# Optimization experiments

Measured on AMD Instinct MI355X. Metric: run time of the kernel, lower is better.

Reference implementation:

```python
import jax, jax.numpy as jnp
import numpy as np

N_USER = 27094
M_SPOT = 42852
N_EDGE = 2_000_000
D_FEAT = 128


def setup_inputs() -> dict:
    key = jax.random.key(0)
    k1, k2, k3, k4 = jax.random.split(key, 4)
    spot_x = jax.random.normal(k1, (M_SPOT, D_FEAT), dtype=jnp.float32)
    user_x = jax.random.normal(k2, (N_USER, D_FEAT), dtype=jnp.float32)
    u_idx = jax.random.randint(k3, (N_EDGE,), 0, N_USER, dtype=jnp.int32)
    s_idx = jax.random.randint(k4, (N_EDGE,), 0, M_SPOT, dtype=jnp.int32)
    user_spot = jnp.stack([u_idx, s_idx], axis=0)  # [2, E]
    return {"spot_x": spot_x, "user_x": user_x, "user_spot": user_spot}


def reference(spot_x, user_x, user_spot):
    u = user_spot[0]  # [E] user index per edge
    s = user_spot[1]  # [E] spot index per edge
    # symmetric GCN normalization: 1/sqrt(deg_u * deg_s) per edge
    user_deg = jnp.bincount(u, length=N_USER)
    spot_deg = jnp.bincount(s, length=M_SPOT)
    div = jnp.sqrt((user_deg[u] * spot_deg[s]).astype(spot_x.dtype))[:, None]  # [E,1]
    # spot -> user aggregation
    source_spot = spot_x[s] / div                                   # [E, D]
    user_out = jax.ops.segment_sum(source_spot, u, num_segments=N_USER)
    # user -> spot aggregation
    source_user = user_x[u] / div                                   # [E, D]
    spot_out = jax.ops.segment_sum(source_user, s, num_segments=M_SPOT)
    return (spot_out, user_out)
```

## Files before the change

kernel.cpp:

```cpp
#include <hip/hip_runtime.h>
#include <stdint.h>


#define NPB_LOG2 6
#define NPB 64
#define MAXB 768
#define PART_CHUNK 2048
#define BH_CHUNK 16384
#define SORT_CAP 8192
#define CSCAN_CH 256

__device__ __forceinline__ ushort f2bf(float f) {
    uint32_t u = __float_as_uint(f);
    return (ushort)((u + 0x7fffu + ((u >> 16) & 1u)) >> 16);
}

__global__ __launch_bounds__(256) void bhist_kernel(
        const int* __restrict__ u, const int* __restrict__ s, int E,
        int nbu, int nbs, int* __restrict__ bd) {
    __shared__ int hist[2 * MAXB];
    const int tid = threadIdx.x;
    const int nb = nbu + nbs;
    const int beg = blockIdx.x * BH_CHUNK;
    const int end = min(beg + BH_CHUNK, E);
    for (int b = tid; b < nb; b += 256) hist[b] = 0;
    __syncthreads();
    for (int i = beg + tid; i < end; i += 256) {
        atomicAdd(&hist[u[i] >> NPB_LOG2], 1);
        atomicAdd(&hist[nbu + (s[i] >> NPB_LOG2)], 1);
    }
    __syncthreads();
    for (int b = tid; b < nb; b += 256) {
        int h = hist[b];
        if (h) atomicAdd(&bd[b], h);
    }
}

__global__ __launch_bounds__(1024) void scan2_kernel(
        const int* __restrict__ bd, int nbu, int nbs,
        int* __restrict__ buoff, int* __restrict__ bsoff,
        int* __restrict__ gcu, int* __restrict__ gcs) {
    __shared__ int wsums[16];
    __shared__ int total;
    const int tid = threadIdx.x, lane = tid & 63, wid = tid >> 6;
    const int n   = blockIdx.x ? nbs : nbu;
    const int* in = blockIdx.x ? (bd + nbu) : bd;
    int* out = blockIdx.x ? bsoff : buoff;
    int* gc  = blockIdx.x ? gcs   : gcu;
    int v = (tid < n) ? in[tid] : 0;
    int x = v;
#pragma unroll
    for (int d = 1; d < 64; d <<= 1) {
        int t = __shfl_up(x, d);
        if (lane >= d) x += t;
    }
    if (lane == 63) wsums[wid] = x;
    __syncthreads();
    if (tid == 0) {
        int run = 0;
#pragma unroll
        for (int w = 0; w < 16; ++w) { int t = wsums[w]; wsums[w] = run; run += t; }
        total = run;
    }
    __syncthreads();
    int excl = wsums[wid] + (x - v);
    if (tid < n) { out[tid] = excl; gc[tid] = excl; }
    if (tid == 0) out[n] = total;
}

__global__ void convert_kernel(const float* __restrict__ x, const float* __restrict__ isd,
                               ushort* __restrict__ xb, int n_rows) {
    int idx = blockIdx.x * blockDim.x + threadIdx.x;
    if (idx >= (n_rows << 6)) return;
    int row = idx >> 6, c = idx & 63;
    float w = isd[row];
    const float* xr = x + ((size_t)row << 7);
    ushort2 o;
    o.x = f2bf(xr[c] * w);
    o.y = f2bf(xr[c + 64] * w);
    *reinterpret_cast<ushort2*>(xb + ((size_t)row << 7) + 2 * c) = o;
}

__global__ __launch_bounds__(256) void part_kernel(
        const int* __restrict__ prim, const int* __restrict__ sec, int E,
        int nb, int* __restrict__ gcur, uint32_t* __restrict__ out) {
    __shared__ int hist[MAXB];
    __shared__ int loff[MAXB];
    __shared__ int gbase[MAXB];
    __shared__ int cur[MAXB];
    __shared__ int wsum[4];
    __shared__ uint32_t sbuf[PART_CHUNK];
    const int tid = threadIdx.x;
    const int lane = tid & 63;
    const int wid = tid >> 6;
    const int beg = blockIdx.x * PART_CHUNK;
    const int end = min(beg + PART_CHUNK, E);
    const int cnt_total = end - beg;
    for (int b = tid; b < nb; b += 256) hist[b] = 0;
    __syncthreads();
    for (int i = beg + tid; i < end; i += 256)
        atomicAdd(&hist[prim[i] >> NPB_LOG2], 1);
    __syncthreads();
    {
        int b0 = tid * 3;
        int h0 = (b0 + 0 < nb) ? hist[b0 + 0] : 0;
        int h1 = (b0 + 1 < nb) ? hist[b0 + 1] : 0;
        int h2 = (b0 + 2 < nb) ? hist[b0 + 2] : 0;
        int tsum = h0 + h1 + h2;
        int x = tsum;
#pragma unroll
        for (int d = 1; d < 64; d <<= 1) {
            int t = __shfl_up(x, d);
            if (lane >= d) x += t;
        }
        if (lane == 63) wsum[wid] = x;
        __syncthreads();
        if (tid == 0) {
            int run = 0;
#pragma unroll
            for (int w = 0; w < 4; ++w) { int t = wsum[w]; wsum[w] = run; run += t; }
        }
        __syncthreads();
        int base = wsum[wid] + (x - tsum);
        if (b0 + 0 < nb) loff[b0 + 0] = base;
        if (b0 + 1 < nb) loff[b0 + 1] = base + h0;
        if (b0 + 2 < nb) loff[b0 + 2] = base + h0 + h1;
    }
    __syncthreads();
    for (int b = tid; b < nb; b += 256) {
        cur[b] = loff[b];
        int c = hist[b];
        gbase[b] = c > 0 ? atomicAdd(&gcur[b], c) : 0;
    }
    __syncthreads();
    for (int i = beg + tid; i < end; i += 256) {
        int p = prim[i], s = sec[i];
        int b = p >> NPB_LOG2;
        int l = atomicAdd(&cur[b], 1);
        sbuf[l] = ((uint32_t)p << 16) | (uint32_t)s;
    }
    __syncthreads();
    for (int k = tid; k < cnt_total; k += 256) {
        uint32_t p = sbuf[k];
        int b = (int)(p >> (16 + NPB_LOG2));
        out[gbase[b] + (k - loff[b])] = p;
    }
}

__global__ __launch_bounds__(256) void bdeg_kernel(
        const uint32_t* __restrict__ buf, const int* __restrict__ boff,
        float* __restrict__ isd, int n_rows) {
    __shared__ int hist[NPB];
    const int tid = threadIdx.x;
    const int jbeg = boff[blockIdx.x];
    const int cnt = boff[blockIdx.x + 1] - jbeg;
    if (tid < NPB) hist[tid] = 0;
    __syncthreads();
    for (int k = tid; k < cnt; k += 256)
        atomicAdd(&hist[(buf[jbeg + k] >> 16) & (NPB - 1)], 1);
    __syncthreads();
    if (tid < NPB) {
        int node = (blockIdx.x << NPB_LOG2) + tid;
        if (node < n_rows) {
            int h = hist[tid];
            isd[node] = h > 0 ? rsqrtf((float)h) : 0.f;
        }
    }
}

__global__ __launch_bounds__(512) void fscan_kernel(
        const ushort* __restrict__ xb, const uint32_t* __restrict__ buf,
        const int* __restrict__ boff, float* __restrict__ isd_out,
        float* __restrict__ out, int n_rows) {
    __shared__ uint32_t sorted[SORT_CAP];
    __shared__ int hist[NPB];
    __shared__ int scur[NPB];
    __shared__ float isdl[NPB];
    const int tid = threadIdx.x;
    const int jbeg = boff[blockIdx.x];
    const int cnt = boff[blockIdx.x + 1] - jbeg;
    if (cnt <= 0) {
        if (tid < NPB) {
            int node = (blockIdx.x << NPB_LOG2) + tid;
            if (node < n_rows) isd_out[node] = 0.f;
        }
        return;
    }
    const bool fits = (cnt <= SORT_CAP);
    if (tid < NPB) hist[tid] = 0;
    __syncthreads();
    for (int k = tid; k < cnt; k += 512)
        atomicAdd(&hist[(buf[jbeg + k] >> 16) & (NPB - 1)], 1);
    __syncthreads();
    if (tid < NPB) {
        int h = hist[tid];
        int x = h;
#pragma unroll
        for (int d = 1; d < 64; d <<= 1) {
            int t = __shfl_up(x, d);
            if (tid >= d) x += t;
        }
        scur[tid] = x - h;
        float iv = h > 0 ? rsqrtf((float)h) : 0.f;
        isdl[tid] = iv;
        int node = (blockIdx.x << NPB_LOG2) + tid;
        if (node < n_rows) isd_out[node] = iv;
    }
    __syncthreads();
    if (fits) {
        for (int k = tid; k < cnt; k += 512) {
            uint32_t p = buf[jbeg + k];
            int slot = atomicAdd(&scur[(p >> 16) & (NPB - 1)], 1);
            sorted[slot] = p;
        }
    }
    __syncthreads();
    const int wid = tid >> 6, lane = tid & 63;
    const int cs = (cnt + 7) >> 3;
    const int beg = wid * cs;
    const int end = min(beg + cs, cnt);
    if (beg >= end) return;
    const int n = end - beg;

#define QLD(i) (fits ? sorted[i] : buf[jbeg + (i)])
#define ROW(pv) (*reinterpret_cast<const uint32_t*>( \
        xb + (((size_t)((pv) & 0xffffu)) << 7) + (lane << 1)))
#define UPX(rv) __uint_as_float((rv) << 16)
#define UPY(rv) __uint_as_float((rv) & 0xffff0000u)
#define FLUSH() do { float w_ = isdl[curd & (NPB - 1)];                    \
        unsafeAtomicAdd(out + ((size_t)curd << 7) + lane, ax * w_);        \
        unsafeAtomicAdd(out + ((size_t)curd << 7) + 64 + lane, ay * w_);   \
        ax = 0.f; ay = 0.f; } while (0)
#define PROC(pv, rv) do { int d_ = (int)((pv) >> 16);                      \
        if (d_ != curd) { FLUSH(); curd = d_; }                            \
        ax += UPX(rv); ay += UPY(rv); } while (0)
#define GRP8(q0,q1,q2,q3,q4,q5,q6,q7, r0,r1,r2,r3,r4,r5,r6,r7) do {        \
    if ((((q0 ^ q7) >> 16) == 0) && ((int)(q0 >> 16) == curd)) {           \
        float sx = ((UPX(r0) + UPX(r1)) + (UPX(r2) + UPX(r3)))             \
                 + ((UPX(r4) + UPX(r5)) + (UPX(r6) + UPX(r7)));            \
        float sy = ((UPY(r0) + UPY(r1)) + (UPY(r2) + UPY(r3)))             \
                 + ((UPY(r4) + UPY(r5)) + (UPY(r6) + UPY(r7)));            \
        ax += sx; ay += sy;                                                \
    } else {                                                               \
        PROC(q0, r0); PROC(q1, r1); PROC(q2, r2); PROC(q3, r3);            \
        PROC(q4, r4); PROC(q5, r5); PROC(q6, r6); PROC(q7, r7);            \
    } } while (0)

    float ax = 0.f, ay = 0.f;
    int curd = (int)(QLD(beg) >> 16);
    int k = 0;
    if (n >= 16) {
        uint32_t a0 = QLD(beg + 0), a1 = QLD(beg + 1), a2 = QLD(beg + 2), a3 = QLD(beg + 3),
                 a4 = QLD(beg + 4), a5 = QLD(beg + 5), a6 = QLD(beg + 6), a7 = QLD(beg + 7);
        uint32_t r0 = ROW(a0), r1 = ROW(a1), r2 = ROW(a2), r3 = ROW(a3),
                 r4 = ROW(a4), r5 = ROW(a5), r6 = ROW(a6), r7 = ROW(a7);
        for (k = 8; k + 8 <= n; k += 8) {
            uint32_t b0 = QLD(beg + k + 0), b1 = QLD(beg + k + 1),
                     b2 = QLD(beg + k + 2), b3 = QLD(beg + k + 3),
                     b4 = QLD(beg + k + 4), b5 = QLD(beg + k + 5),
                     b6 = QLD(beg + k + 6), b7 = QLD(beg + k + 7);
            uint32_t s0 = ROW(b0), s1 = ROW(b1), s2 = ROW(b2), s3 = ROW(b3),
                     s4 = ROW(b4), s5 = ROW(b5), s6 = ROW(b6), s7 = ROW(b7);
            GRP8(a0,a1,a2,a3,a4,a5,a6,a7, r0,r1,r2,r3,r4,r5,r6,r7);
            a0 = b0; a1 = b1; a2 = b2; a3 = b3; a4 = b4; a5 = b5; a6 = b6; a7 = b7;
            r0 = s0; r1 = s1; r2 = s2; r3 = s3; r4 = s4; r5 = s5; r6 = s6; r7 = s7;
        }
        GRP8(a0,a1,a2,a3,a4,a5,a6,a7, r0,r1,r2,r3,r4,r5,r6,r7);
    }
    for (; k < n; ++k) {
        uint32_t p = QLD(beg + k);
        uint32_t r = ROW(p);
        PROC(p, r);
    }
    FLUSH();
#undef GRP8
#undef PROC
#undef FLUSH
#undef UPY
#undef UPX
#undef ROW
#undef QLD
}


__global__ __launch_bounds__(1024) void scan_kernel(const int* __restrict__ in,
                                                    int* __restrict__ out, int n) {
    __shared__ int ws[17];
    const int tid  = threadIdx.x;
    const int lane = tid & 63;
    const int wid  = tid >> 6;
    int carry = 0;
    for (int base = 0; base < n; base += 4096) {
        int idx = base + tid * 4;
        int v0 = (idx + 0 < n) ? in[idx + 0] : 0;
        int v1 = (idx + 1 < n) ? in[idx + 1] : 0;
        int v2 = (idx + 2 < n) ? in[idx + 2] : 0;
        int v3 = (idx + 3 < n) ? in[idx + 3] : 0;
        int tsum = v0 + v1 + v2 + v3;
        int x = tsum;
#pragma unroll
        for (int d = 1; d < 64; d <<= 1) {
            int t = __shfl_up(x, d);
            if (lane >= d) x += t;
        }
        if (lane == 63) ws[wid] = x;
        __syncthreads();
        if (tid == 0) {
            int run = carry;
#pragma unroll
            for (int w = 0; w < 16; ++w) { int t = ws[w]; ws[w] = run; run += t; }
            carry = run;
        }
        __syncthreads();
        int excl = ws[wid] + (x - tsum);
        if (idx + 0 < n) out[idx + 0] = excl; excl += v0;
        if (idx + 1 < n) out[idx + 1] = excl; excl += v1;
        if (idx + 2 < n) out[idx + 2] = excl; excl += v2;
        if (idx + 3 < n) out[idx + 3] = excl;
        __syncthreads();
    }
    if (tid == 0) out[n] = carry;
}

__global__ void deg_kernel(const int* __restrict__ u, const int* __restrict__ s,
                           int E, int* __restrict__ udeg, int* __restrict__ sdeg) {
    int i = blockIdx.x * blockDim.x + threadIdx.x;
    int i4 = i * 4;
    if (i4 + 3 < E) {
        int4 a = *reinterpret_cast<const int4*>(u + i4);
        int4 b = *reinterpret_cast<const int4*>(s + i4);
        atomicAdd(&udeg[a.x], 1); atomicAdd(&udeg[a.y], 1);
        atomicAdd(&udeg[a.z], 1); atomicAdd(&udeg[a.w], 1);
        atomicAdd(&sdeg[b.x], 1); atomicAdd(&sdeg[b.y], 1);
        atomicAdd(&sdeg[b.z], 1); atomicAdd(&sdeg[b.w], 1);
    } else {
        for (int k = i4; k < E; ++k) {
            atomicAdd(&udeg[u[k]], 1);
            atomicAdd(&sdeg[s[k]], 1);
        }
    }
}

__global__ void init_isd_kernel(const int* __restrict__ udeg, const int* __restrict__ sdeg,
                                float* __restrict__ isd_u, float* __restrict__ isd_s,
                                int n_user, int m_spot) {
    int i = blockIdx.x * blockDim.x + threadIdx.x;
    if (i < n_user) { int d = udeg[i]; isd_u[i] = d > 0 ? rsqrtf((float)d) : 0.f; }
    if (i < m_spot) { int d = sdeg[i]; isd_s[i] = d > 0 ? rsqrtf((float)d) : 0.f; }
}

__global__ void breduce_kernel(const int* __restrict__ udeg, const int* __restrict__ sdeg,
                               int N, int M, int nbu, int nbs,
                               int* __restrict__ bdu, int* __restrict__ bds) {
    const int w = (blockIdx.x * blockDim.x + threadIdx.x) >> 6;
    const int lane = threadIdx.x & 63;
    if (w >= nbu + nbs) return;
    int v;
    if (w < nbu) {
        int i = (w << NPB_LOG2) + lane;
        v = (i < N) ? udeg[i] : 0;
    } else {
        int i = ((w - nbu) << NPB_LOG2) + lane;
        v = (i < M) ? sdeg[i] : 0;
    }
#pragma unroll
    for (int d = 32; d >= 1; d >>= 1) v += __shfl_down(v, d);
    if (lane == 0) {
        if (w < nbu) bdu[w] = v; else bds[w - nbu] = v;
    }
}

__global__ void gcur3_init_kernel(const int* __restrict__ buoff, const int* __restrict__ bsoff,
                                  int* __restrict__ gcu, int* __restrict__ gcs,
                                  int nbu, int nbs) {
    int i = blockIdx.x * blockDim.x + threadIdx.x;
    if (i < nbu) gcu[i] = buoff[i];
    if (i < nbs) gcs[i] = bsoff[i];
}

__global__ void gcur_init_kernel(const int* __restrict__ uoff, const int* __restrict__ soff,
                                 int* __restrict__ gcur_u, int* __restrict__ gcur_s,
                                 int nbu, int nbs) {
    int i = blockIdx.x * blockDim.x + threadIdx.x;
    if (i < nbu) gcur_u[i] = uoff[i << NPB_LOG2];
    if (i < nbs) gcur_s[i] = soff[i << NPB_LOG2];
}

__global__ __launch_bounds__(256) void bsort_kernel(
        const uint32_t* __restrict__ packed, const int* __restrict__ noff,
        int nodes, int* __restrict__ csr) {
    __shared__ int cur[NPB];
    const int tid = threadIdx.x;
    const int ubase = blockIdx.x << NPB_LOG2;
    const int nin = min(NPB, nodes - ubase);
    if (tid < nin) cur[tid] = noff[ubase + tid];
    __syncthreads();
    const int jbeg = noff[ubase];
    const int jend = noff[ubase + nin];
    for (int j = jbeg + tid; j < jend; j += 256) {
        uint32_t p = packed[j];
        int local = (int)(p >> 16) - ubase;
        int slot = atomicAdd(&cur[local], 1);
        csr[slot] = (int)(p & 0xffffu);
    }
}

__global__ __launch_bounds__(256) void bsort3_kernel(
        uint32_t* __restrict__ buf, const int* __restrict__ boff,
        float* __restrict__ isd, int n_rows) {
    __shared__ uint32_t stage[SORT_CAP];
    __shared__ int hist[NPB];
    __shared__ int cur[NPB];
    const int tid = threadIdx.x;
    const int jbeg = boff[blockIdx.x];
    const int cnt = boff[blockIdx.x + 1] - jbeg;
    const bool fits = (cnt <= SORT_CAP);
    if (tid < NPB) hist[tid] = 0;
    __syncthreads();
    for (int k = tid; k < cnt; k += 256) {
        uint32_t p = buf[jbeg + k];
        if (fits) stage[k] = p;
        atomicAdd(&hist[(p >> 16) & (NPB - 1)], 1);
    }
    __syncthreads();
    if (tid < NPB) {
        int h = hist[tid];
        int x = h;
#pragma unroll
        for (int d = 1; d < 64; d <<= 1) {
            int t = __shfl_up(x, d);
            if (tid >= d) x += t;
        }
        cur[tid] = x - h;
        int node = (blockIdx.x << NPB_LOG2) + tid;
        if (node < n_rows) isd[node] = h > 0 ? rsqrtf((float)h) : 0.f;
    }
    __syncthreads();
    if (fits) {
        for (int k = tid; k < cnt; k += 256) {
            uint32_t p = stage[k];
            int slot = atomicAdd(&cur[(p >> 16) & (NPB - 1)], 1);
            buf[jbeg + slot] = p;
        }
    }
}

__global__ __launch_bounds__(256) void cscan_kernel(
        const ushort* __restrict__ xb, const uint32_t* __restrict__ packed, int E,
        const float* __restrict__ isd, float* __restrict__ out) {
    const int lane = threadIdx.x & 63;
    const int wave = (blockIdx.x << 2) + (threadIdx.x >> 6);
    const int base = wave * CSCAN_CH;
    if (base >= E) return;
    const int n = min(CSCAN_CH, E - base);
    const uint32_t* pp = packed + base;
    float ax = 0.f, ay = 0.f;
    int cur = (int)(pp[0] >> 16);

#define ROW(pv) (*reinterpret_cast<const uint32_t*>( \
        xb + (((size_t)((pv) & 0xffffu)) << 7) + (lane << 1)))
#define PROC(pv, rv) do {                                                  \
        int d_ = (int)((pv) >> 16);                                        \
        if (d_ != cur) {                                                   \
            float w_ = isd[cur];                                           \
            unsafeAtomicAdd(out + ((size_t)cur << 7) + lane, ax * w_);     \
            unsafeAtomicAdd(out + ((size_t)cur << 7) + 64 + lane, ay * w_);\
            ax = 0.f; ay = 0.f; cur = d_;                                  \
        }                                                                  \
        ax += __uint_as_float((rv) << 16);                                 \
        ay += __uint_as_float((rv) & 0xffff0000u);                         \
    } while (0)

    int k = 0;
    if (n >= 16) {
        uint4 Pa = *reinterpret_cast<const uint4*>(pp);
        uint4 Pb = *reinterpret_cast<const uint4*>(pp + 4);
        uint32_t r0 = ROW(Pa.x), r1 = ROW(Pa.y), r2 = ROW(Pa.z), r3 = ROW(Pa.w);
        uint32_t r4 = ROW(Pb.x), r5 = ROW(Pb.y), r6 = ROW(Pb.z), r7 = ROW(Pb.w);
        for (k = 8; k + 8 <= n; k += 8) {
            uint4 Na = *reinterpret_cast<const uint4*>(pp + k);
            uint4 Nb = *reinterpret_cast<const uint4*>(pp + k + 4);
            PROC(Pa.x, r0); PROC(Pa.y, r1); PROC(Pa.z, r2); PROC(Pa.w, r3);
            PROC(Pb.x, r4); PROC(Pb.y, r5); PROC(Pb.z, r6); PROC(Pb.w, r7);
            r0 = ROW(Na.x); r1 = ROW(Na.y); r2 = ROW(Na.z); r3 = ROW(Na.w);
            r4 = ROW(Nb.x); r5 = ROW(Nb.y); r6 = ROW(Nb.z); r7 = ROW(Nb.w);
            Pa = Na; Pb = Nb;
        }
        PROC(Pa.x, r0); PROC(Pa.y, r1); PROC(Pa.z, r2); PROC(Pa.w, r3);
        PROC(Pb.x, r4); PROC(Pb.y, r5); PROC(Pb.z, r6); PROC(Pb.w, r7);
    }
    for (; k < n; ++k) {
        uint32_t p = pp[k];
        uint32_t r = ROW(p);
        PROC(p, r);
    }
    float w = isd[cur];
    unsafeAtomicAdd(out + ((size_t)cur << 7) + lane, ax * w);
    unsafeAtomicAdd(out + ((size_t)cur << 7) + 64 + lane, ay * w);
#undef PROC
#undef ROW
}

__global__ __launch_bounds__(256) void gather_kernel(const float* __restrict__ x_src,
                                                     const int* __restrict__ nbr,
                                                     const int* __restrict__ off,
                                                     const float* __restrict__ isd_dst,
                                                     const float* __restrict__ isd_src,
                                                     float* __restrict__ out, int n_rows) {
    const int lane = threadIdx.x & 63;
    const int row  = blockIdx.x * 4 + (threadIdx.x >> 6);
    if (row >= n_rows) return;
    const int jbeg = off[row];
    const int jend = off[row + 1];
    const float wd = isd_dst[row];
    float ax = 0.f, ay = 0.f;
    if (jbeg < jend) {
        int sidx = nbr[jbeg];
        for (int j = jbeg; j < jend; ++j) {
            int snext = (j + 1 < jend) ? nbr[j + 1] : 0;
            float w = wd * isd_src[sidx];
            const float2 v = *reinterpret_cast<const float2*>(x_src + (size_t)sidx * 128 + lane * 2);
            ax = fmaf(v.x, w, ax);
            ay = fmaf(v.y, w, ay);
            sidx = snext;
        }
    }
    float2 r; r.x = ax; r.y = ay;
    *reinterpret_cast<float2*>(out + (size_t)row * 128 + lane * 2) = r;
}

__global__ __launch_bounds__(256) void scatter_kernel(const float* __restrict__ spot_x,
                                                      const float* __restrict__ user_x,
                                                      const int* __restrict__ u,
                                                      const int* __restrict__ s, int E,
                                                      const float* __restrict__ isd_u,
                                                      const float* __restrict__ isd_s,
                                                      float* __restrict__ spot_out,
                                                      float* __restrict__ user_out) {
    const int lane = threadIdx.x & 63;
    const int e = blockIdx.x * 4 + (threadIdx.x >> 6);
    if (e >= E) return;
    const int uu = u[e], ss = s[e];
    const float w = isd_u[uu] * isd_s[ss];
    const float2 sv = *reinterpret_cast<const float2*>(spot_x + (size_t)ss * 128 + lane * 2);
    const float2 uv = *reinterpret_cast<const float2*>(user_x + (size_t)uu * 128 + lane * 2);
    atomicAdd(&user_out[(size_t)uu * 128 + lane * 2 + 0], sv.x * w);
    atomicAdd(&user_out[(size_t)uu * 128 + lane * 2 + 1], sv.y * w);
    atomicAdd(&spot_out[(size_t)ss * 128 + lane * 2 + 0], uv.x * w);
    atomicAdd(&spot_out[(size_t)ss * 128 + lane * 2 + 1], uv.y * w);
}

static inline char* align256(char* p) {
    return (char*)(((uintptr_t)p + 255u) & ~(uintptr_t)255u);
}

extern "C" void kernel_launch(void* const* d_in, const int* in_sizes, int n_in,
                              void* d_out, int out_size, void* d_ws, size_t ws_size,
                              hipStream_t stream) {
    const float* spot_x = (const float*)d_in[0];
    const float* user_x = (const float*)d_in[1];
    const int*   edges  = (const int*)d_in[2];
    const int M = in_sizes[0] / 128;
    const int N = in_sizes[1] / 128;
    const int E = in_sizes[2] / 2;
    const int* u = edges;
    const int* s = edges + E;
    float* spot_out = (float*)d_out;
    float* user_out = (float*)d_out + (size_t)M * 128;

    const int nbu = (N + NPB - 1) / NPB;
    const int nbs = (M + NPB - 1) / NPB;
    const int nm = (N > M) ? N : M;
    const int gpart = (E + PART_CHUNK - 1) / PART_CHUNK;
    const int gscan = ((E + CSCAN_CH - 1) / CSCAN_CH + 3) / 4;

    {
        char* ws = (char*)d_ws;
        float*    isd_u = (float*)ws; ws = align256(ws + sizeof(float) * (size_t)N);
        float*    isd_s = (float*)ws; ws = align256(ws + sizeof(float) * (size_t)M);
        int*      bd    = (int*)ws;   ws = align256(ws + sizeof(int) * (size_t)(nbu + nbs));
        int*      buoff = (int*)ws;   ws = align256(ws + sizeof(int) * (size_t)(nbu + 1));
        int*      bsoff = (int*)ws;   ws = align256(ws + sizeof(int) * (size_t)(nbs + 1));
        int*      gcu   = (int*)ws;   ws = align256(ws + sizeof(int) * (size_t)nbu);
        int*      gcs   = (int*)ws;   ws = align256(ws + sizeof(int) * (size_t)nbs);
        uint32_t* bufU  = (uint32_t*)ws; ws = align256(ws + sizeof(uint32_t) * (size_t)E);
        uint32_t* bufS  = (uint32_t*)ws; ws = align256(ws + sizeof(uint32_t) * (size_t)E);
        ushort*   xb    = (ushort*)ws;
        size_t fast_needed = (size_t)(ws - (char*)d_ws) + sizeof(ushort) * ((size_t)nm * 128);

        if (fast_needed <= ws_size && nbu <= MAXB && nbs <= MAXB) {
            hipMemsetAsync(bd, 0, sizeof(int) * (size_t)(nbu + nbs), stream);
            hipMemsetAsync(d_out, 0, sizeof(float) * (size_t)out_size, stream);
            bhist_kernel<<<(E + BH_CHUNK - 1) / BH_CHUNK, 256, 0, stream>>>(
                u, s, E, nbu, nbs, bd);
            scan2_kernel<<<2, 1024, 0, stream>>>(bd, nbu, nbs, buoff, bsoff, gcu, gcs);
            part_kernel<<<gpart, 256, 0, stream>>>(u, s, E, nbu, gcu, bufU);
            part_kernel<<<gpart, 256, 0, stream>>>(s, u, E, nbs, gcs, bufS);
            bdeg_kernel<<<nbs, 256, 0, stream>>>(bufS, bsoff, isd_s, M);
            convert_kernel<<<((M << 6) + 255) / 256, 256, 0, stream>>>(spot_x, isd_s, xb, M);
            fscan_kernel<<<nbu, 512, 0, stream>>>(xb, bufU, buoff, isd_u, user_out, N);
            convert_kernel<<<((N << 6) + 255) / 256, 256, 0, stream>>>(user_x, isd_u, xb, N);
            fscan_kernel<<<nbs, 512, 0, stream>>>(xb, bufS, bsoff, isd_s, spot_out, M);
            return;
        }
    }

    char* ws = (char*)d_ws;
    int*      udeg  = (int*)ws;  ws = align256(ws + sizeof(int) * (size_t)(N + M));
    int*      sdeg  = udeg + N;
    float*    isd_u = (float*)ws; ws = align256(ws + sizeof(float) * (size_t)N);
    float*    isd_s = (float*)ws; ws = align256(ws + sizeof(float) * (size_t)M);
    size_t fallback_needed = (size_t)(ws - (char*)d_ws);
    int*      uoff  = (int*)ws;  ws = align256(ws + sizeof(int) * (size_t)(N + 1));
    int*      soff  = (int*)ws;  ws = align256(ws + sizeof(int) * (size_t)(M + 1));
    int*      bdu   = (int*)ws;  ws = align256(ws + sizeof(int) * (size_t)nbu);
    int*      bds   = (int*)ws;  ws = align256(ws + sizeof(int) * (size_t)nbs);
    int*      buoff = (int*)ws;  ws = align256(ws + sizeof(int) * (size_t)(nbu + 1));
    int*      bsoff = (int*)ws;  ws = align256(ws + sizeof(int) * (size_t)(nbs + 1));
    int*      gcu   = (int*)ws;  ws = align256(ws + sizeof(int) * (size_t)nbu);
    int*      gcs   = (int*)ws;  ws = align256(ws + sizeof(int) * (size_t)nbs);
    uint32_t* bufA  = (uint32_t*)ws; ws = align256(ws + sizeof(uint32_t) * (size_t)E);
    char* mark = ws;
    ushort*   xbs   = (ushort*)mark;
    ushort*   xbu   = (ushort*)align256(mark + sizeof(ushort) * ((size_t)M * 128));
    size_t new_needed = (size_t)((char*)xbu - (char*)d_ws) + sizeof(ushort) * ((size_t)N * 128);
    int*      bufB  = (int*)mark;
    size_t old_needed = (size_t)(mark - (char*)d_ws) + sizeof(int) * (size_t)E;

    hipMemsetAsync(udeg, 0, sizeof(int) * (size_t)(N + M), stream);
    deg_kernel<<<(E / 4 + 255) / 256, 256, 0, stream>>>(u, s, E, udeg, sdeg);
    init_isd_kernel<<<(nm + 255) / 256, 256, 0, stream>>>(udeg, sdeg, isd_u, isd_s, N, M);

    if (new_needed <= ws_size && nbu <= MAXB && nbs <= MAXB) {
        convert_kernel<<<((M << 6) + 255) / 256, 256, 0, stream>>>(spot_x, isd_s, xbs, M);
        convert_kernel<<<((N << 6) + 255) / 256, 256, 0, stream>>>(user_x, isd_u, xbu, N);
        breduce_kernel<<<((nbu + nbs) * 64 + 255) / 256, 256, 0, stream>>>(
            udeg, sdeg, N, M, nbu, nbs, bdu, bds);
        scan_kernel<<<1, 1024, 0, stream>>>(bdu, buoff, nbu);
        scan_kernel<<<1, 1024, 0, stream>>>(bds, bsoff, nbs);
        gcur3_init_kernel<<<(nbs + nbu + 255) / 256, 256, 0, stream>>>(
            buoff, bsoff, gcu, gcs, nbu, nbs);
        hipMemsetAsync(d_out, 0, sizeof(float) * (size_t)out_size, stream);
        part_kernel<<<gpart, 256, 0, stream>>>(u, s, E, nbu, gcu, bufA);
        bsort3_kernel<<<nbu, 256, 0, stream>>>(bufA, buoff, isd_u, N);
        cscan_kernel<<<gscan, 256, 0, stream>>>(xbs, bufA, E, isd_u, user_out);
        part_kernel<<<gpart, 256, 0, stream>>>(s, u, E, nbs, gcs, bufA);
        bsort3_kernel<<<nbs, 256, 0, stream>>>(bufA, bsoff, isd_s, M);
        cscan_kernel<<<gscan, 256, 0, stream>>>(xbu, bufA, E, isd_s, spot_out);
    } else if (old_needed <= ws_size && nbu <= MAXB && nbs <= MAXB) {
        scan_kernel<<<1, 1024, 0, stream>>>(udeg, uoff, N);
        scan_kernel<<<1, 1024, 0, stream>>>(sdeg, soff, M);
        gcur_init_kernel<<<(nbs + nbu + 255) / 256, 256, 0, stream>>>(uoff, soff, gcu, gcs, nbu, nbs);
        part_kernel<<<gpart, 256, 0, stream>>>(u, s, E, nbu, gcu, bufA);
        bsort_kernel<<<nbu, 256, 0, stream>>>(bufA, uoff, N, bufB);
        gather_kernel<<<(N + 3) / 4, 256, 0, stream>>>(spot_x, bufB, uoff,
                                                       isd_u, isd_s, user_out, N);
        part_kernel<<<gpart, 256, 0, stream>>>(s, u, E, nbs, gcs, bufA);
        bsort_kernel<<<nbs, 256, 0, stream>>>(bufA, soff, M, bufB);
        gather_kernel<<<(M + 3) / 4, 256, 0, stream>>>(user_x, bufB, soff,
                                                       isd_s, isd_u, spot_out, M);
    } else if (fallback_needed <= ws_size) {
        hipMemsetAsync(d_out, 0, sizeof(float) * (size_t)out_size, stream);
        scatter_kernel<<<((size_t)E + 3) / 4, 256, 0, stream>>>(spot_x, user_x, u, s, E,
                                                                isd_u, isd_s, spot_out, user_out);
    }
}
```

Before: 274.9 us.

## Merge both aggregation directions into single fused degree and segmented-scan launches

Adds bdeg2 and fscan2 kernels that cover the user and spot partitions in one grid each, so the two directions no longer run as separate back-to-back launches. Both bf16 feature tables are converted up front into separate buffers. fscan2 sorts only 16-bit neighbour indices in shared memory, which lets bucket capacity grow, and computes each destination row per wave with a plain store instead of atomics. Older fallback paths are removed and the GRP8 unrolling in fscan is simplified. The fused path needs more workspace, and falls back to the old two-pass sequence when that space is not available.

```diff
diff --git a/kernel.cpp b/kernel.cpp
--- a/kernel.cpp
+++ b/kernel.cpp
@@ -8,7 +8,7 @@
 #define PART_CHUNK 2048
 #define BH_CHUNK 16384
 #define SORT_CAP 8192
-#define CSCAN_CH 256
+#define SORT2_CAP 16384
 
 __device__ __forceinline__ ushort f2bf(float f) {
     uint32_t u = __float_as_uint(f);
@@ -147,6 +147,151 @@
     }
 }
 
+__global__ __launch_bounds__(256) void bdeg2_kernel(
+        const uint32_t* __restrict__ bufU, const uint32_t* __restrict__ bufS,
+        const int* __restrict__ buoff, const int* __restrict__ bsoff, int nbu,
+        float* __restrict__ isd_u, float* __restrict__ isd_s, int N, int M) {
+    __shared__ int hist[NPB];
+    const int tid = threadIdx.x;
+    const int b = blockIdx.x;
+    const uint32_t* buf; const int* boff; float* isd; int n_rows; int bb;
+    if (b < nbu) { buf = bufU; boff = buoff; isd = isd_u; n_rows = N; bb = b; }
+    else         { buf = bufS; boff = bsoff; isd = isd_s; n_rows = M; bb = b - nbu; }
+    const int jbeg = boff[bb];
+    const int cnt = boff[bb + 1] - jbeg;
+    if (tid < NPB) hist[tid] = 0;
+    __syncthreads();
+    for (int k = tid; k < cnt; k += 256)
+        atomicAdd(&hist[(buf[jbeg + k] >> 16) & (NPB - 1)], 1);
+    __syncthreads();
+    if (tid < NPB) {
+        int node = (bb << NPB_LOG2) + tid;
+        if (node < n_rows) {
+            int h = hist[tid];
+            isd[node] = h > 0 ? rsqrtf((float)h) : 0.f;
+        }
+    }
+}
+
+__global__ __launch_bounds__(512) void fscan2_kernel(
+        const ushort* __restrict__ xbs, const ushort* __restrict__ xbu,
+        const uint32_t* __restrict__ bufU, const uint32_t* __restrict__ bufS,
+        const int* __restrict__ buoff, const int* __restrict__ bsoff, int nbu,
+        float* __restrict__ user_out, float* __restrict__ spot_out) {
+    __shared__ ushort srt[SORT2_CAP];
+    __shared__ int hist[NPB];
+    __shared__ int scur[NPB];
+    __shared__ float isdl[NPB];
+    const int tid = threadIdx.x;
+    const int b = blockIdx.x;
+    const ushort* xb; const uint32_t* buf; const int* boff; float* out; int bb;
+    if (b < nbu) { xb = xbs; buf = bufU; boff = buoff; out = user_out; bb = b; }
+    else         { xb = xbu; buf = bufS; boff = bsoff; out = spot_out; bb = b - nbu; }
+    const int jbeg = boff[bb];
+    const int cnt = boff[bb + 1] - jbeg;
+    if (cnt <= 0) return;
+    const bool fits = (cnt <= SORT2_CAP);
+    if (tid < NPB) hist[tid] = 0;
+    __syncthreads();
+    for (int k = tid; k < cnt; k += 512)
+        atomicAdd(&hist[(buf[jbeg + k] >> 16) & (NPB - 1)], 1);
+    __syncthreads();
+    if (tid < NPB) {
+        int h = hist[tid];
+        int x = h;
+#pragma unroll
+        for (int d = 1; d < 64; d <<= 1) {
+            int t = __shfl_up(x, d);
+            if (tid >= d) x += t;
+        }
+        scur[tid] = x - h;
+        isdl[tid] = h > 0 ? rsqrtf((float)h) : 0.f;
+    }
+    __syncthreads();
+    if (fits) {
+        for (int k = tid; k < cnt; k += 512) {
+            uint32_t p = buf[jbeg + k];
+            int slot = atomicAdd(&scur[(p >> 16) & (NPB - 1)], 1);
+            srt[slot] = (ushort)p;
+        }
+    }
+    __syncthreads();
+    const int wid = tid >> 6, lane = tid & 63;
+    const int rowbase = bb << NPB_LOG2;
+
+#define ROWX(sv) (*reinterpret_cast<const uint32_t*>( \
+        xb + (((size_t)(sv)) << 7) + (lane << 1)))
+#define UPX(rv) __uint_as_float((rv) << 16)
+#define UPY(rv) __uint_as_float((rv) & 0xffff0000u)
+
+    if (fits) {
+        for (int ld = wid; ld < NPB; ld += 8) {
+            const int deg = hist[ld];
+            if (!deg) continue;
+            const int off0 = scur[ld] - deg;
+            const float w = isdl[ld];
+            float ax = 0.f, ay = 0.f;
+            int j = 0;
+            if (deg >= 16) {
+                ushort c0 = srt[off0+0], c1 = srt[off0+1], c2 = srt[off0+2], c3 = srt[off0+3],
+                       c4 = srt[off0+4], c5 = srt[off0+5], c6 = srt[off0+6], c7 = srt[off0+7];
+                uint32_t r0 = ROWX(c0), r1 = ROWX(c1), r2 = ROWX(c2), r3 = ROWX(c3),
+                         r4 = ROWX(c4), r5 = ROWX(c5), r6 = ROWX(c6), r7 = ROWX(c7);
+                for (j = 8; j + 8 <= deg; j += 8) {
+                    const int q = off0 + j;
+                    ushort n0 = srt[q+0], n1 = srt[q+1], n2 = srt[q+2], n3 = srt[q+3],
+                           n4 = srt[q+4], n5 = srt[q+5], n6 = srt[q+6], n7 = srt[q+7];
+                    uint32_t s0 = ROWX(n0), s1 = ROWX(n1), s2 = ROWX(n2), s3 = ROWX(n3),
+                             s4 = ROWX(n4), s5 = ROWX(n5), s6 = ROWX(n6), s7 = ROWX(n7);
+                    ax += ((UPX(r0) + UPX(r1)) + (UPX(r2) + UPX(r3)))
+                        + ((UPX(r4) + UPX(r5)) + (UPX(r6) + UPX(r7)));
+                    ay += ((UPY(r0) + UPY(r1)) + (UPY(r2) + UPY(r3)))
+                        + ((UPY(r4) + UPY(r5)) + (UPY(r6) + UPY(r7)));
+                    r0 = s0; r1 = s1; r2 = s2; r3 = s3;
+                    r4 = s4; r5 = s5; r6 = s6; r7 = s7;
+                }
+                ax += ((UPX(r0) + UPX(r1)) + (UPX(r2) + UPX(r3)))
+                    + ((UPX(r4) + UPX(r5)) + (UPX(r6) + UPX(r7)));
+                ay += ((UPY(r0) + UPY(r1)) + (UPY(r2) + UPY(r3)))
+                    + ((UPY(r4) + UPY(r5)) + (UPY(r6) + UPY(r7)));
+            }
+            for (; j < deg; ++j) {
+                uint32_t r = ROWX(srt[off0 + j]);
+                ax += UPX(r); ay += UPY(r);
+            }
+            const size_t ro = ((size_t)(rowbase + ld)) << 7;
+            out[ro + lane]      = ax * w;
+            out[ro + 64 + lane] = ay * w;
+        }
+    } else {
+        const int cs = (cnt + 7) >> 3;
+        const int beg = wid * cs;
+        const int end = min(beg + cs, cnt);
+        if (beg >= end) return;
+        float ax = 0.f, ay = 0.f;
+        int curd = (int)(buf[jbeg + beg] >> 16);
+        for (int k = beg; k < end; ++k) {
+            uint32_t p = buf[jbeg + k];
+            int d_ = (int)(p >> 16);
+            if (d_ != curd) {
+                float w_ = isdl[curd & (NPB - 1)];
+                unsafeAtomicAdd(out + ((size_t)curd << 7) + lane, ax * w_);
+                unsafeAtomicAdd(out + ((size_t)curd << 7) + 64 + lane, ay * w_);
+                ax = 0.f; ay = 0.f; curd = d_;
+            }
+            uint32_t r = ROWX((ushort)p);
+            ax += UPX(r); ay += UPY(r);
+        }
+        float w_ = isdl[curd & (NPB - 1)];
+        unsafeAtomicAdd(out + ((size_t)curd << 7) + lane, ax * w_);
+        unsafeAtomicAdd(out + ((size_t)curd << 7) + 64 + lane, ay * w_);
+    }
+#undef UPY
+#undef UPX
+#undef ROWX
+}
+
+
 __global__ __launch_bounds__(256) void bdeg_kernel(
         const uint32_t* __restrict__ buf, const int* __restrict__ boff,
         float* __restrict__ isd, int n_rows) {
@@ -220,62 +365,29 @@
     const int beg = wid * cs;
     const int end = min(beg + cs, cnt);
     if (beg >= end) return;
-    const int n = end - beg;
 
 #define QLD(i) (fits ? sorted[i] : buf[jbeg + (i)])
 #define ROW(pv) (*reinterpret_cast<const uint32_t*>( \
         xb + (((size_t)((pv) & 0xffffu)) << 7) + (lane << 1)))
 #define UPX(rv) __uint_as_float((rv) << 16)
 #define UPY(rv) __uint_as_float((rv) & 0xffff0000u)
-#define FLUSH() do { float w_ = isdl[curd & (NPB - 1)];                    \
-        unsafeAtomicAdd(out + ((size_t)curd << 7) + lane, ax * w_);        \
-        unsafeAtomicAdd(out + ((size_t)curd << 7) + 64 + lane, ay * w_);   \
-        ax = 0.f; ay = 0.f; } while (0)
-#define PROC(pv, rv) do { int d_ = (int)((pv) >> 16);                      \
-        if (d_ != curd) { FLUSH(); curd = d_; }                            \
-        ax += UPX(rv); ay += UPY(rv); } while (0)
-#define GRP8(q0,q1,q2,q3,q4,q5,q6,q7, r0,r1,r2,r3,r4,r5,r6,r7) do {        \
-    if ((((q0 ^ q7) >> 16) == 0) && ((int)(q0 >> 16) == curd)) {           \
-        float sx = ((UPX(r0) + UPX(r1)) + (UPX(r2) + UPX(r3)))             \
-                 + ((UPX(r4) + UPX(r5)) + (UPX(r6) + UPX(r7)));            \
-        float sy = ((UPY(r0) + UPY(r1)) + (UPY(r2) + UPY(r3)))             \
-                 + ((UPY(r4) + UPY(r5)) + (UPY(r6) + UPY(r7)));            \
-        ax += sx; ay += sy;                                                \
-    } else {                                                               \
-        PROC(q0, r0); PROC(q1, r1); PROC(q2, r2); PROC(q3, r3);            \
-        PROC(q4, r4); PROC(q5, r5); PROC(q6, r6); PROC(q7, r7);            \
-    } } while (0)
-
     float ax = 0.f, ay = 0.f;
     int curd = (int)(QLD(beg) >> 16);
-    int k = 0;
-    if (n >= 16) {
-        uint32_t a0 = QLD(beg + 0), a1 = QLD(beg + 1), a2 = QLD(beg + 2), a3 = QLD(beg + 3),
-                 a4 = QLD(beg + 4), a5 = QLD(beg + 5), a6 = QLD(beg + 6), a7 = QLD(beg + 7);
-        uint32_t r0 = ROW(a0), r1 = ROW(a1), r2 = ROW(a2), r3 = ROW(a3),
-                 r4 = ROW(a4), r5 = ROW(a5), r6 = ROW(a6), r7 = ROW(a7);
-        for (k = 8; k + 8 <= n; k += 8) {
-            uint32_t b0 = QLD(beg + k + 0), b1 = QLD(beg + k + 1),
-                     b2 = QLD(beg + k + 2), b3 = QLD(beg + k + 3),
-                     b4 = QLD(beg + k + 4), b5 = QLD(beg + k + 5),
-                     b6 = QLD(beg + k + 6), b7 = QLD(beg + k + 7);
-            uint32_t s0 = ROW(b0), s1 = ROW(b1), s2 = ROW(b2), s3 = ROW(b3),
-                     s4 = ROW(b4), s5 = ROW(b5), s6 = ROW(b6), s7 = ROW(b7);
-            GRP8(a0,a1,a2,a3,a4,a5,a6,a7, r0,r1,r2,r3,r4,r5,r6,r7);
-            a0 = b0; a1 = b1; a2 = b2; a3 = b3; a4 = b4; a5 = b5; a6 = b6; a7 = b7;
-            r0 = s0; r1 = s1; r2 = s2; r3 = s3; r4 = s4; r5 = s5; r6 = s6; r7 = s7;
-        }
-        GRP8(a0,a1,a2,a3,a4,a5,a6,a7, r0,r1,r2,r3,r4,r5,r6,r7);
-    }
-    for (; k < n; ++k) {
-        uint32_t p = QLD(beg + k);
+    for (int k = beg; k < end; ++k) {
+        uint32_t p = QLD(k);
+        int d_ = (int)(p >> 16);
+        if (d_ != curd) {
+            float w_ = isdl[curd & (NPB - 1)];
+            unsafeAtomicAdd(out + ((size_t)curd << 7) + lane, ax * w_);
+            unsafeAtomicAdd(out + ((size_t)curd << 7) + 64 + lane, ay * w_);
+            ax = 0.f; ay = 0.f; curd = d_;
+        }
         uint32_t r = ROW(p);
-        PROC(p, r);
-    }
-    FLUSH();
-#undef GRP8
-#undef PROC
-#undef FLUSH
+        ax += UPX(r); ay += UPY(r);
+    }
+    float w_ = isdl[curd & (NPB - 1)];
+    unsafeAtomicAdd(out + ((size_t)curd << 7) + lane, ax * w_);
+    unsafeAtomicAdd(out + ((size_t)curd << 7) + 64 + lane, ay * w_);
 #undef UPY
 #undef UPX
 #undef ROW
@@ -283,61 +395,12 @@
 }
 
 
-__global__ __launch_bounds__(1024) void scan_kernel(const int* __restrict__ in,
-                                                    int* __restrict__ out, int n) {
-    __shared__ int ws[17];
-    const int tid  = threadIdx.x;
-    const int lane = tid & 63;
-    const int wid  = tid >> 6;
-    int carry = 0;
-    for (int base = 0; base < n; base += 4096) {
-        int idx = base + tid * 4;
-        int v0 = (idx + 0 < n) ? in[idx + 0] : 0;
-        int v1 = (idx + 1 < n) ? in[idx + 1] : 0;
-        int v2 = (idx + 2 < n) ? in[idx + 2] : 0;
-        int v3 = (idx + 3 < n) ? in[idx + 3] : 0;
-        int tsum = v0 + v1 + v2 + v3;
-        int x = tsum;
-#pragma unroll
-        for (int d = 1; d < 64; d <<= 1) {
-            int t = __shfl_up(x, d);
-            if (lane >= d) x += t;
-        }
-        if (lane == 63) ws[wid] = x;
-        __syncthreads();
-        if (tid == 0) {
-            int run = carry;
-#pragma unroll
-            for (int w = 0; w < 16; ++w) { int t = ws[w]; ws[w] = run; run += t; }
-            carry = run;
-        }
-        __syncthreads();
-        int excl = ws[wid] + (x - tsum);
-        if (idx + 0 < n) out[idx + 0] = excl; excl += v0;
-        if (idx + 1 < n) out[idx + 1] = excl; excl += v1;
-        if (idx + 2 < n) out[idx + 2] = excl; excl += v2;
-        if (idx + 3 < n) out[idx + 3] = excl;
-        __syncthreads();
-    }
-    if (tid == 0) out[n] = carry;
-}
-
 __global__ void deg_kernel(const int* __restrict__ u, const int* __restrict__ s,
                            int E, int* __restrict__ udeg, int* __restrict__ sdeg) {
     int i = blockIdx.x * blockDim.x + threadIdx.x;
-    int i4 = i * 4;
-    if (i4 + 3 < E) {
-        int4 a = *reinterpret_cast<const int4*>(u + i4);
-        int4 b = *reinterpret_cast<const int4*>(s + i4);
-        atomicAdd(&udeg[a.x], 1); atomicAdd(&udeg[a.y], 1);
-        atomicAdd(&udeg[a.z], 1); atomicAdd(&udeg[a.w], 1);
-        atomicAdd(&sdeg[b.x], 1); atomicAdd(&sdeg[b.y], 1);
-        atomicAdd(&sdeg[b.z], 1); atomicAdd(&sdeg[b.w], 1);
-    } else {
-        for (int k = i4; k < E; ++k) {
-            atomicAdd(&udeg[u[k]], 1);
-            atomicAdd(&sdeg[s[k]], 1);
-        }
+    if (i < E) {
+        atomicAdd(&udeg[u[i]], 1);
+        atomicAdd(&sdeg[s[i]], 1);
     }
 }
 
@@ -347,186 +410,6 @@
     int i = blockIdx.x * blockDim.x + threadIdx.x;
     if (i < n_user) { int d = udeg[i]; isd_u[i] = d > 0 ? rsqrtf((float)d) : 0.f; }
     if (i < m_spot) { int d = sdeg[i]; isd_s[i] = d > 0 ? rsqrtf((float)d) : 0.f; }
-}
-
-__global__ void breduce_kernel(const int* __restrict__ udeg, const int* __restrict__ sdeg,
-                               int N, int M, int nbu, int nbs,
-                               int* __restrict__ bdu, int* __restrict__ bds) {
-    const int w = (blockIdx.x * blockDim.x + threadIdx.x) >> 6;
-    const int lane = threadIdx.x & 63;
-    if (w >= nbu + nbs) return;
-    int v;
-    if (w < nbu) {
-        int i = (w << NPB_LOG2) + lane;
-        v = (i < N) ? udeg[i] : 0;
-    } else {
-        int i = ((w - nbu) << NPB_LOG2) + lane;
-        v = (i < M) ? sdeg[i] : 0;
-    }
-#pragma unroll
-    for (int d = 32; d >= 1; d >>= 1) v += __shfl_down(v, d);
-    if (lane == 0) {
-        if (w < nbu) bdu[w] = v; else bds[w - nbu] = v;
-    }
-}
-
-__global__ void gcur3_init_kernel(const int* __restrict__ buoff, const int* __restrict__ bsoff,
-                                  int* __restrict__ gcu, int* __restrict__ gcs,
-                                  int nbu, int nbs) {
-    int i = blockIdx.x * blockDim.x + threadIdx.x;
-    if (i < nbu) gcu[i] = buoff[i];
-    if (i < nbs) gcs[i] = bsoff[i];
-}
-
-__global__ void gcur_init_kernel(const int* __restrict__ uoff, const int* __restrict__ soff,
-                                 int* __restrict__ gcur_u, int* __restrict__ gcur_s,
-                                 int nbu, int nbs) {
-    int i = blockIdx.x * blockDim.x + threadIdx.x;
-    if (i < nbu) gcur_u[i] = uoff[i << NPB_LOG2];
-    if (i < nbs) gcur_s[i] = soff[i << NPB_LOG2];
-}
-
-__global__ __launch_bounds__(256) void bsort_kernel(
-        const uint32_t* __restrict__ packed, const int* __restrict__ noff,
-        int nodes, int* __restrict__ csr) {
-    __shared__ int cur[NPB];
-    const int tid = threadIdx.x;
-    const int ubase = blockIdx.x << NPB_LOG2;
-    const int nin = min(NPB, nodes - ubase);
-    if (tid < nin) cur[tid] = noff[ubase + tid];
-    __syncthreads();
-    const int jbeg = noff[ubase];
-    const int jend = noff[ubase + nin];
-    for (int j = jbeg + tid; j < jend; j += 256) {
-        uint32_t p = packed[j];
-        int local = (int)(p >> 16) - ubase;
-        int slot = atomicAdd(&cur[local], 1);
-        csr[slot] = (int)(p & 0xffffu);
-    }
-}
-
-__global__ __launch_bounds__(256) void bsort3_kernel(
-        uint32_t* __restrict__ buf, const int* __restrict__ boff,
-        float* __restrict__ isd, int n_rows) {
-    __shared__ uint32_t stage[SORT_CAP];
-    __shared__ int hist[NPB];
-    __shared__ int cur[NPB];
-    const int tid = threadIdx.x;
-    const int jbeg = boff[blockIdx.x];
-    const int cnt = boff[blockIdx.x + 1] - jbeg;
-    const bool fits = (cnt <= SORT_CAP);
-    if (tid < NPB) hist[tid] = 0;
-    __syncthreads();
-    for (int k = tid; k < cnt; k += 256) {
-        uint32_t p = buf[jbeg + k];
-        if (fits) stage[k] = p;
-        atomicAdd(&hist[(p >> 16) & (NPB - 1)], 1);
-    }
-    __syncthreads();
-    if (tid < NPB) {
-        int h = hist[tid];
-        int x = h;
-#pragma unroll
-        for (int d = 1; d < 64; d <<= 1) {
-            int t = __shfl_up(x, d);
-            if (tid >= d) x += t;
-        }
-        cur[tid] = x - h;
-        int node = (blockIdx.x << NPB_LOG2) + tid;
-        if (node < n_rows) isd[node] = h > 0 ? rsqrtf((float)h) : 0.f;
-    }
-    __syncthreads();
-    if (fits) {
-        for (int k = tid; k < cnt; k += 256) {
-            uint32_t p = stage[k];
-            int slot = atomicAdd(&cur[(p >> 16) & (NPB - 1)], 1);
-            buf[jbeg + slot] = p;
-        }
-    }
-}
-
-__global__ __launch_bounds__(256) void cscan_kernel(
-        const ushort* __restrict__ xb, const uint32_t* __restrict__ packed, int E,
-        const float* __restrict__ isd, float* __restrict__ out) {
-    const int lane = threadIdx.x & 63;
-    const int wave = (blockIdx.x << 2) + (threadIdx.x >> 6);
-    const int base = wave * CSCAN_CH;
-    if (base >= E) return;
-    const int n = min(CSCAN_CH, E - base);
-    const uint32_t* pp = packed + base;
-    float ax = 0.f, ay = 0.f;
-    int cur = (int)(pp[0] >> 16);
-
-#define ROW(pv) (*reinterpret_cast<const uint32_t*>( \
-        xb + (((size_t)((pv) & 0xffffu)) << 7) + (lane << 1)))
-#define PROC(pv, rv) do {                                                  \
-        int d_ = (int)((pv) >> 16);                                        \
-        if (d_ != cur) {                                                   \
-            float w_ = isd[cur];                                           \
-            unsafeAtomicAdd(out + ((size_t)cur << 7) + lane, ax * w_);     \
-            unsafeAtomicAdd(out + ((size_t)cur << 7) + 64 + lane, ay * w_);\
-            ax = 0.f; ay = 0.f; cur = d_;                                  \
-        }                                                                  \
-        ax += __uint_as_float((rv) << 16);                                 \
-        ay += __uint_as_float((rv) & 0xffff0000u);                         \
-    } while (0)
-
-    int k = 0;
-    if (n >= 16) {
-        uint4 Pa = *reinterpret_cast<const uint4*>(pp);
-        uint4 Pb = *reinterpret_cast<const uint4*>(pp + 4);
-        uint32_t r0 = ROW(Pa.x), r1 = ROW(Pa.y), r2 = ROW(Pa.z), r3 = ROW(Pa.w);
-        uint32_t r4 = ROW(Pb.x), r5 = ROW(Pb.y), r6 = ROW(Pb.z), r7 = ROW(Pb.w);
-        for (k = 8; k + 8 <= n; k += 8) {
-            uint4 Na = *reinterpret_cast<const uint4*>(pp + k);
-            uint4 Nb = *reinterpret_cast<const uint4*>(pp + k + 4);
-            PROC(Pa.x, r0); PROC(Pa.y, r1); PROC(Pa.z, r2); PROC(Pa.w, r3);
-            PROC(Pb.x, r4); PROC(Pb.y, r5); PROC(Pb.z, r6); PROC(Pb.w, r7);
-            r0 = ROW(Na.x); r1 = ROW(Na.y); r2 = ROW(Na.z); r3 = ROW(Na.w);
-            r4 = ROW(Nb.x); r5 = ROW(Nb.y); r6 = ROW(Nb.z); r7 = ROW(Nb.w);
-            Pa = Na; Pb = Nb;
-        }
-        PROC(Pa.x, r0); PROC(Pa.y, r1); PROC(Pa.z, r2); PROC(Pa.w, r3);
-        PROC(Pb.x, r4); PROC(Pb.y, r5); PROC(Pb.z, r6); PROC(Pb.w, r7);
-    }
-    for (; k < n; ++k) {
-        uint32_t p = pp[k];
-        uint32_t r = ROW(p);
-        PROC(p, r);
-    }
-    float w = isd[cur];
-    unsafeAtomicAdd(out + ((size_t)cur << 7) + lane, ax * w);
-    unsafeAtomicAdd(out + ((size_t)cur << 7) + 64 + lane, ay * w);
-#undef PROC
-#undef ROW
-}
-
-__global__ __launch_bounds__(256) void gather_kernel(const float* __restrict__ x_src,
-                                                     const int* __restrict__ nbr,
-                                                     const int* __restrict__ off,
-                                                     const float* __restrict__ isd_dst,
-                                                     const float* __restrict__ isd_src,
-                                                     float* __restrict__ out, int n_rows) {
-    const int lane = threadIdx.x & 63;
-    const int row  = blockIdx.x * 4 + (threadIdx.x >> 6);
-    if (row >= n_rows) return;
-    const int jbeg = off[row];
-    const int jend = off[row + 1];
-    const float wd = isd_dst[row];
-    float ax = 0.f, ay = 0.f;
-    if (jbeg < jend) {
-        int sidx = nbr[jbeg];
-        for (int j = jbeg; j < jend; ++j) {
-            int snext = (j + 1 < jend) ? nbr[j + 1] : 0;
-            float w = wd * isd_src[sidx];
-            const float2 v = *reinterpret_cast<const float2*>(x_src + (size_t)sidx * 128 + lane * 2);
-            ax = fmaf(v.x, w, ax);
-            ay = fmaf(v.y, w, ay);
-            sidx = snext;
-        }
-    }
-    float2 r; r.x = ax; r.y = ay;
-    *reinterpret_cast<float2*>(out + (size_t)row * 128 + lane * 2) = r;
 }
 
 __global__ __launch_bounds__(256) void scatter_kernel(const float* __restrict__ spot_x,
@@ -572,96 +455,64 @@
     const int nbs = (M + NPB - 1) / NPB;
     const int nm = (N > M) ? N : M;
     const int gpart = (E + PART_CHUNK - 1) / PART_CHUNK;
-    const int gscan = ((E + CSCAN_CH - 1) / CSCAN_CH + 3) / 4;
-
-    {
-        char* ws = (char*)d_ws;
-        float*    isd_u = (float*)ws; ws = align256(ws + sizeof(float) * (size_t)N);
-        float*    isd_s = (float*)ws; ws = align256(ws + sizeof(float) * (size_t)M);
-        int*      bd    = (int*)ws;   ws = align256(ws + sizeof(int) * (size_t)(nbu + nbs));
-        int*      buoff = (int*)ws;   ws = align256(ws + sizeof(int) * (size_t)(nbu + 1));
-        int*      bsoff = (int*)ws;   ws = align256(ws + sizeof(int) * (size_t)(nbs + 1));
-        int*      gcu   = (int*)ws;   ws = align256(ws + sizeof(int) * (size_t)nbu);
-        int*      gcs   = (int*)ws;   ws = align256(ws + sizeof(int) * (size_t)nbs);
-        uint32_t* bufU  = (uint32_t*)ws; ws = align256(ws + sizeof(uint32_t) * (size_t)E);
-        uint32_t* bufS  = (uint32_t*)ws; ws = align256(ws + sizeof(uint32_t) * (size_t)E);
-        ushort*   xb    = (ushort*)ws;
-        size_t fast_needed = (size_t)(ws - (char*)d_ws) + sizeof(ushort) * ((size_t)nm * 128);
-
-        if (fast_needed <= ws_size && nbu <= MAXB && nbs <= MAXB) {
-            hipMemsetAsync(bd, 0, sizeof(int) * (size_t)(nbu + nbs), stream);
-            hipMemsetAsync(d_out, 0, sizeof(float) * (size_t)out_size, stream);
-            bhist_kernel<<<(E + BH_CHUNK - 1) / BH_CHUNK, 256, 0, stream>>>(
-                u, s, E, nbu, nbs, bd);
-            scan2_kernel<<<2, 1024, 0, stream>>>(bd, nbu, nbs, buoff, bsoff, gcu, gcs);
-            part_kernel<<<gpart, 256, 0, stream>>>(u, s, E, nbu, gcu, bufU);
-            part_kernel<<<gpart, 256, 0, stream>>>(s, u, E, nbs, gcs, bufS);
+
+    char* ws = (char*)d_ws;
+    float*    isd_u = (float*)ws; ws = align256(ws + sizeof(float) * (size_t)N);
+    float*    isd_s = (float*)ws; ws = align256(ws + sizeof(float) * (size_t)M);
+    int*      bd    = (int*)ws;   ws = align256(ws + sizeof(int) * (size_t)(nbu + nbs));
+    int*      buoff = (int*)ws;   ws = align256(ws + sizeof(int) * (size_t)(nbu + 1));
+    int*      bsoff = (int*)ws;   ws = align256(ws + sizeof(int) * (size_t)(nbs + 1));
+    int*      gcu   = (int*)ws;   ws = align256(ws + sizeof(int) * (size_t)nbu);
+    int*      gcs   = (int*)ws;   ws = align256(ws + sizeof(int) * (size_t)nbs);
+    uint32_t* bufU  = (uint32_t*)ws; ws = align256(ws + sizeof(uint32_t) * (size_t)E);
+    uint32_t* bufS  = (uint32_t*)ws; ws = align256(ws + sizeof(uint32_t) * (size_t)E);
+    ushort*   xbs   = (ushort*)ws;
+    ushort*   xbu   = (ushort*)align256((char*)xbs + sizeof(ushort) * ((size_t)M * 128));
+    size_t tierA_needed = (size_t)((char*)xbu - (char*)d_ws)
+                        + sizeof(ushort) * ((size_t)N * 128);
+    size_t tierB_needed = (size_t)((char*)xbs - (char*)d_ws)
+                        + sizeof(ushort) * ((size_t)nm * 128);
+
+    if (tierB_needed <= ws_size && nbu <= MAXB && nbs <= MAXB) {
+        hipMemsetAsync(bd, 0, sizeof(int) * (size_t)(nbu + nbs), stream);
+        hipMemsetAsync(d_out, 0, sizeof(float) * (size_t)out_size, stream);
+        bhist_kernel<<<(E + BH_CHUNK - 1) / BH_CHUNK, 256, 0, stream>>>(
+            u, s, E, nbu, nbs, bd);
+        scan2_kernel<<<2, 1024, 0, stream>>>(bd, nbu, nbs, buoff, bsoff, gcu, gcs);
+        part_kernel<<<gpart, 256, 0, stream>>>(u, s, E, nbu, gcu, bufU);
+        part_kernel<<<gpart, 256, 0, stream>>>(s, u, E, nbs, gcs, bufS);
+        if (tierA_needed <= ws_size) {
+            bdeg2_kernel<<<nbu + nbs, 256, 0, stream>>>(
+                bufU, bufS, buoff, bsoff, nbu, isd_u, isd_s, N, M);
+            convert_kernel<<<((M << 6) + 255) / 256, 256, 0, stream>>>(spot_x, isd_s, xbs, M);
+            convert_kernel<<<((N << 6) + 255) / 256, 256, 0, stream>>>(user_x, isd_u, xbu, N);
+            fscan2_kernel<<<nbu + nbs, 512, 0, stream>>>(
+                xbs, xbu, bufU, bufS, buoff, bsoff, nbu, user_out, spot_out);
+        } else {
+            ushort* xb = xbs;
             bdeg_kernel<<<nbs, 256, 0, stream>>>(bufS, bsoff, isd_s, M);
             convert_kernel<<<((M << 6) + 255) / 256, 256, 0, stream>>>(spot_x, isd_s, xb, M);
             fscan_kernel<<<nbu, 512, 0, stream>>>(xb, bufU, buoff, isd_u, user_out, N);
             convert_kernel<<<((N << 6) + 255) / 256, 256, 0, stream>>>(user_x, isd_u, xb, N);
             fscan_kernel<<<nbs, 512, 0, stream>>>(xb, bufS, bsoff, isd_s, spot_out, M);
-            return;
-        }
-    }
-
-    char* ws = (char*)d_ws;
-    int*      udeg  = (int*)ws;  ws = align256(ws + sizeof(int) * (size_t)(N + M));
-    int*      sdeg  = udeg + N;
-    float*    isd_u = (float*)ws; ws = align256(ws + sizeof(float) * (size_t)N);
-    float*    isd_s = (float*)ws; ws = align256(ws + sizeof(float) * (size_t)M);
-    size_t fallback_needed = (size_t)(ws - (char*)d_ws);
-    int*      uoff  = (int*)ws;  ws = align256(ws + sizeof(int) * (size_t)(N + 1));
-    int*      soff  = (int*)ws;  ws = align256(ws + sizeof(int) * (size_t)(M + 1));
-    int*      bdu   = (int*)ws;  ws = align256(ws + sizeof(int) * (size_t)nbu);
-    int*      bds   = (int*)ws;  ws = align256(ws + sizeof(int) * (size_t)nbs);
-    int*      buoff = (int*)ws;  ws = align256(ws + sizeof(int) * (size_t)(nbu + 1));
-    int*      bsoff = (int*)ws;  ws = align256(ws + sizeof(int) * (size_t)(nbs + 1));
-    int*      gcu   = (int*)ws;  ws = align256(ws + sizeof(int) * (size_t)nbu);
-    int*      gcs   = (int*)ws;  ws = align256(ws + sizeof(int) * (size_t)nbs);
-    uint32_t* bufA  = (uint32_t*)ws; ws = align256(ws + sizeof(uint32_t) * (size_t)E);
-    char* mark = ws;
-    ushort*   xbs   = (ushort*)mark;
-    ushort*   xbu   = (ushort*)align256(mark + sizeof(ushort) * ((size_t)M * 128));
-    size_t new_needed = (size_t)((char*)xbu - (char*)d_ws) + sizeof(ushort) * ((size_t)N * 128);
-    int*      bufB  = (int*)mark;
-    size_t old_needed = (size_t)(mark - (char*)d_ws) + sizeof(int) * (size_t)E;
-
-    hipMemsetAsync(udeg, 0, sizeof(int) * (size_t)(N + M), stream);
-    deg_kernel<<<(E / 4 + 255) / 256, 256, 0, stream>>>(u, s, E, udeg, sdeg);
-    init_isd_kernel<<<(nm + 255) / 256, 256, 0, stream>>>(udeg, sdeg, isd_u, isd_s, N, M);
-
-    if (new_needed <= ws_size && nbu <= MAXB && nbs <= MAXB) {
-        convert_kernel<<<((M << 6) + 255) / 256, 256, 0, stream>>>(spot_x, isd_s, xbs, M);
-        convert_kernel<<<((N << 6) + 255) / 256, 256, 0, stream>>>(user_x, isd_u, xbu, N);
-        breduce_kernel<<<((nbu + nbs) * 64 + 255) / 256, 256, 0, stream>>>(
-            udeg, sdeg, N, M, nbu, nbs, bdu, bds);
-        scan_kernel<<<1, 1024, 0, stream>>>(bdu, buoff, nbu);
-        scan_kernel<<<1, 1024, 0, stream>>>(bds, bsoff, nbs);
-        gcur3_init_kernel<<<(nbs + nbu + 255) / 256, 256, 0, stream>>>(
-            buoff, bsoff, gcu, gcs, nbu, nbs);
-        hipMemsetAsync(d_out, 0, sizeof(float) * (size_t)out_size, stream);
-        part_kernel<<<gpart, 256, 0, stream>>>(u, s, E, nbu, gcu, bufA);
-        bsort3_kernel<<<nbu, 256, 0, stream>>>(bufA, buoff, isd_u, N);
-        cscan_kernel<<<gscan, 256, 0, stream>>>(xbs, bufA, E, isd_u, user_out);
-        part_kernel<<<gpart, 256, 0, stream>>>(s, u, E, nbs, gcs, bufA);
-        bsort3_kernel<<<nbs, 256, 0, stream>>>(bufA, bsoff, isd_s, M);
-        cscan_kernel<<<gscan, 256, 0, stream>>>(xbu, bufA, E, isd_s, spot_out);
-    } else if (old_needed <= ws_size && nbu <= MAXB && nbs <= MAXB) {
-        scan_kernel<<<1, 1024, 0, stream>>>(udeg, uoff, N);
-        scan_kernel<<<1, 1024, 0, stream>>>(sdeg, soff, M);
-        gcur_init_kernel<<<(nbs + nbu + 255) / 256, 256, 0, stream>>>(uoff, soff, gcu, gcs, nbu, nbs);
-        part_kernel<<<gpart, 256, 0, stream>>>(u, s, E, nbu, gcu, bufA);
-        bsort_kernel<<<nbu, 256, 0, stream>>>(bufA, uoff, N, bufB);
-        gather_kernel<<<(N + 3) / 4, 256, 0, stream>>>(spot_x, bufB, uoff,
-                                                       isd_u, isd_s, user_out, N);
-        part_kernel<<<gpart, 256, 0, stream>>>(s, u, E, nbs, gcs, bufA);
-        bsort_kernel<<<nbs, 256, 0, stream>>>(bufA, soff, M, bufB);
-        gather_kernel<<<(M + 3) / 4, 256, 0, stream>>>(user_x, bufB, soff,
-                                                       isd_s, isd_u, spot_out, M);
-    } else if (fallback_needed <= ws_size) {
-        hipMemsetAsync(d_out, 0, sizeof(float) * (size_t)out_size, stream);
-        scatter_kernel<<<((size_t)E + 3) / 4, 256, 0, stream>>>(spot_x, user_x, u, s, E,
-                                                                isd_u, isd_s, spot_out, user_out);
-    }
-}
+        }
+        return;
+    }
+
+    {
+        char* w2 = (char*)d_ws;
+        int*   udeg2  = (int*)w2;   w2 += sizeof(int) * (size_t)N;
+        int*   sdeg2  = (int*)w2;   w2 += sizeof(int) * (size_t)M;
+        float* isd_u2 = (float*)w2; w2 += sizeof(float) * (size_t)N;
+        float* isd_s2 = (float*)w2; w2 += sizeof(float) * (size_t)M;
+        if ((size_t)(w2 - (char*)d_ws) <= ws_size) {
+            hipMemsetAsync(udeg2, 0, sizeof(int) * (size_t)(N + M), stream);
+            deg_kernel<<<(E + 255) / 256, 256, 0, stream>>>(u, s, E, udeg2, sdeg2);
+            init_isd_kernel<<<(nm + 255) / 256, 256, 0, stream>>>(
+                udeg2, sdeg2, isd_u2, isd_s2, N, M);
+            hipMemsetAsync(d_out, 0, sizeof(float) * (size_t)out_size, stream);
+            scatter_kernel<<<((size_t)E + 3) / 4, 256, 0, stream>>>(
+                spot_x, user_x, u, s, E, isd_u2, isd_s2, spot_out, user_out);
+        }
+    }
+}
```

Result: slower. 282.0 us (+2.6%).
